# Kernel tuning notes

Measured on AMD Instinct MI355X. Metric: run time of the kernel, lower is better.

The kernel has to match this reference:

```python
import jax, jax.numpy as jnp
import numpy as np

N_NODES = 50000
N_EDGES = 800000
IN_DIM = 128
HID = 128
N_GRAPHS = 256
N_CLASSES = 2
ALPHA = 0.2  # leaky relu slope
EPS_BN = 1e-5


def setup_inputs() -> dict:
    key = jax.random.key(0)
    ks = jax.random.split(key, 24)
    adjacency = jax.random.randint(ks[0], (2, N_EDGES), 0, N_NODES, dtype=jnp.int32)
    input_feature = jax.random.normal(ks[1], (N_NODES, IN_DIM), dtype=jnp.float32)
    graph_indicator = jnp.sort(jax.random.randint(ks[2], (N_NODES,), 0, N_GRAPHS, dtype=jnp.int32))
    labels = jax.random.randint(ks[3], (N_GRAPHS,), 0, N_CLASSES, dtype=jnp.int64)
    s = 0.05
    params = {
        'W1': jax.random.normal(ks[4], (IN_DIM, HID), jnp.float32) * s,
        'a1': jax.random.normal(ks[5], (2 * HID,), jnp.float32) * s,
        'bn2_g': jnp.ones((HID,), jnp.float32),
        'bn2_b': jnp.zeros((HID,), jnp.float32),
        'W2': jax.random.normal(ks[6], (HID, HID), jnp.float32) * s,
        'a2': jax.random.normal(ks[7], (2 * HID,), jnp.float32) * s,
        'bn3_g': jnp.ones((HID,), jnp.float32),
        'bn3_b': jnp.zeros((HID,), jnp.float32),
        'W3': jax.random.normal(ks[8], (HID, HID), jnp.float32) * s,
        'a3': jax.random.normal(ks[9], (2 * HID,), jnp.float32) * s,
        'fc1_w': jax.random.normal(ks[10], (HID, 2 * HID), jnp.float32) * s,
        'fc1_b': jnp.zeros((2 * HID,), jnp.float32),
        'fc2_w': jax.random.normal(ks[11], (2 * HID, HID), jnp.float32) * s,
        'fc2_b': jnp.zeros((HID,), jnp.float32),
        'fc3_w': jax.random.normal(ks[12], (HID, N_CLASSES), jnp.float32) * s,
        'fc3_b': jnp.zeros((N_CLASSES,), jnp.float32),
    }
    return dict(adjacency=adjacency, input_feature=input_feature,
                graph_indicator=graph_indicator, labels=labels, **params)


def _batchnorm(x, g, b):
    # training-mode BatchNorm1d over node dim (biased variance)
    mu = jnp.mean(x, axis=0)
    var = jnp.mean((x - mu) ** 2, axis=0)
    return (x - mu) * jax.lax.rsqrt(var + EPS_BN) * g + b


def _sp_gat(x, src, dst, W, a):
    # pyGAT SpGraphAttentionLayer (dropout disabled / eval mode)
    h = x @ W                                # [N, F]
    F = h.shape[1]
    e_src = h @ a[:F]                        # [N]
    e_dst = h @ a[F:]                        # [N]
    e = e_src[src] + e_dst[dst]              # [E]
    ee = jnp.exp(-jax.nn.leaky_relu(e, ALPHA))
    rowsum = jax.ops.segment_sum(ee, src, num_segments=N_NODES)          # [N]
    num = jax.ops.segment_sum(ee[:, None] * h[dst], src, num_segments=N_NODES)  # [N, F]
    h_prime = num / (rowsum[:, None] + 1e-16)
    return jax.nn.elu(h_prime)


def reference(adjacency, input_feature, graph_indicator, labels,
              W1, a1, bn2_g, bn2_b, W2, a2, bn3_g, bn3_b, W3, a3,
              fc1_w, fc1_b, fc2_w, fc2_b, fc3_w, fc3_b):
    src, dst = adjacency[0], adjacency[1]
    # bn1 output is discarded in the original forward
    x = _sp_gat(input_feature, src, dst, W1, a1)
    x = _batchnorm(x, bn2_g, bn2_b)
    x = _sp_gat(x, src, dst, W2, a2)
    x = _batchnorm(x, bn3_g, bn3_b)
    x = _sp_gat(x, src, dst, W3, a3)
    # pooling_sum_4tensor: per-graph sum pooling
    pooled = jax.ops.segment_sum(x, graph_indicator, num_segments=N_GRAPHS)  # [G, F]
    x = jax.nn.relu(pooled @ fc1_w + fc1_b)
    x = jax.nn.relu(x @ fc2_w + fc2_b)
    logits = x @ fc3_w + fc3_b
    return logits
```

## Files before the change

### kernel.cpp

```cpp
#include <hip/hip_runtime.h>
#include <hip/hip_bf16.h>

#define N_NODES 50000
#define N_EDGES 800000
#define FD 128
#define N_GRAPHS 256
#define NPART 6250

typedef unsigned short u16;
typedef short bf16x8 __attribute__((ext_vector_type(8)));
typedef float f32x4 __attribute__((ext_vector_type(4)));

__device__ __forceinline__ u16 f2bf(float v) {
    __hip_bfloat16 h = __float2bfloat16(v);
    union { __hip_bfloat16 hh; u16 u; } c; c.hh = h; return c.u;
}
__device__ __forceinline__ float bf2f(u16 r) {
    return __uint_as_float(((unsigned int)r) << 16);
}

__global__ __launch_bounds__(256) void count_deg_part_k(const int* __restrict__ src,
                                                        int* __restrict__ cnt, int E) {
    int part = blockIdx.x & 7;
    int lo = part * NPART, hi = lo + NPART;
    int stride = (gridDim.x >> 3) * 256;
    for (int e = (blockIdx.x >> 3) * 256 + threadIdx.x; e < E; e += stride) {
        int s = src[e];
        if (s >= lo && s < hi) atomicAdd(&cnt[s], 1);
    }
}

__global__ __launch_bounds__(256) void fill_csr_part_k(const int* __restrict__ src,
                                                       const int* __restrict__ dst,
                                                       int* __restrict__ cur,
                                                       int2* __restrict__ epak, int E) {
    int part = blockIdx.x & 7;
    int lo = part * NPART, hi = lo + NPART;
    int stride = (gridDim.x >> 3) * 256;
    for (int e = (blockIdx.x >> 3) * 256 + threadIdx.x; e < E; e += stride) {
        int s = src[e];
        if (s >= lo && s < hi) {
            int p = atomicAdd(&cur[s], 1);
            epak[p].x = dst[e];
        }
    }
}

__global__ __launch_bounds__(256) void scan1_k(const int* __restrict__ cnt,
                                               int* __restrict__ bsum, int M) {
    int i = blockIdx.x * 256 + threadIdx.x;
    int v = (i < M) ? cnt[i] : 0;
    __shared__ int l[256];
    l[threadIdx.x] = v;
    __syncthreads();
    for (int s = 128; s > 0; s >>= 1) {
        if (threadIdx.x < s) l[threadIdx.x] += l[threadIdx.x + s];
        __syncthreads();
    }
    if (threadIdx.x == 0) bsum[blockIdx.x] = l[0];
}

__global__ __launch_bounds__(256) void scan2_k(int* __restrict__ bsum, int NB) {
    int tid = threadIdx.x;
    int v = (tid < NB) ? bsum[tid] : 0;
    __shared__ int l[256];
    l[tid] = v;
    __syncthreads();
    for (int off = 1; off < 256; off <<= 1) {
        int t = (tid >= off) ? l[tid - off] : 0;
        __syncthreads();
        l[tid] += t;
        __syncthreads();
    }
    if (tid < NB) bsum[tid] = l[tid] - v;
}

__global__ __launch_bounds__(256) void scan3_k(const int* __restrict__ cnt,
                                               const int* __restrict__ bsum,
                                               int* __restrict__ offs,
                                               int* __restrict__ cur, int M) {
    int i = blockIdx.x * 256 + threadIdx.x;
    int tid = threadIdx.x;
    int v = (i < M) ? cnt[i] : 0;
    __shared__ int l[256];
    l[tid] = v;
    __syncthreads();
    for (int off = 1; off < 256; off <<= 1) {
        int t = (tid >= off) ? l[tid - off] : 0;
        __syncthreads();
        l[tid] += t;
        __syncthreads();
    }
    int excl = l[tid] - v + bsum[blockIdx.x];
    if (i < M) { offs[i] = excl; cur[i] = excl; }
    if (i == M - 1) offs[M] = excl + v;
}

__global__ __launch_bounds__(256) void cvt_in_k(const float* __restrict__ X,
                                                u16* __restrict__ Xb, int n4) {
    int i = blockIdx.x * 256 + threadIdx.x;
    if (i < n4) {
        float4 v = ((const float4*)X)[i];
        ushort4 o;
        o.x = f2bf(v.x); o.y = f2bf(v.y); o.z = f2bf(v.z); o.w = f2bf(v.w);
        ((ushort4*)Xb)[i] = o;
    }
}

__global__ __launch_bounds__(128) void wprep_k(const float* __restrict__ W,
                                               const float* __restrict__ scale,
                                               const float* __restrict__ shift,
                                               u16* __restrict__ Wt,
                                               float* __restrict__ cvec) {
    int n = blockIdx.x, k = threadIdx.x;
    float w = W[(size_t)k * FD + n];
    Wt[(size_t)n * FD + k] = f2bf(scale[k] * w);
    __shared__ float l[128];
    l[k] = shift[k] * w;
    __syncthreads();
    for (int s = 64; s > 0; s >>= 1) {
        if (k < s) l[k] += l[k + s];
        __syncthreads();
    }
    if (k == 0) cvec[n] = l[0];
}

__global__ __launch_bounds__(256) void gemm_mfma_k(const u16* __restrict__ Xb,
                                                   const u16* __restrict__ Wt,
                                                   const float* __restrict__ cvec,
                                                   const float* __restrict__ avec,
                                                   u16* __restrict__ Hb,
                                                   float* __restrict__ es,
                                                   float* __restrict__ ed, int M) {
    __shared__ u16 As[64][136];
    __shared__ u16 Bs[128][136];
    __shared__ float sa_s[128], sa_d[128], cv[128];
    int tid = threadIdx.x;
    if (tid < 128) { sa_s[tid] = avec[tid]; sa_d[tid] = avec[128 + tid]; cv[tid] = cvec[tid]; }
    int row0 = blockIdx.x * 64;
    {
        int n = tid >> 1, k0 = (tid & 1) * 64;
        const uint4* s = (const uint4*)(Wt + (size_t)n * FD + k0);
#pragma unroll
        for (int u = 0; u < 8; u++) *(uint4*)&Bs[n][k0 + u * 8] = s[u];
    }
    {
        int r = tid >> 2, k0 = (tid & 3) * 32;
        int grow = row0 + r;
        if (grow < M) {
            const uint4* s = (const uint4*)(Xb + (size_t)grow * FD + k0);
#pragma unroll
            for (int u = 0; u < 4; u++) *(uint4*)&As[r][k0 + u * 8] = s[u];
        } else {
            uint4 z = make_uint4(0, 0, 0, 0);
#pragma unroll
            for (int u = 0; u < 4; u++) *(uint4*)&As[r][k0 + u * 8] = z;
        }
    }
    __syncthreads();

    int wave = tid >> 6, lane = tid & 63;
    int quad = lane >> 4, n16 = lane & 15;
    int rbase = wave * 16;
    f32x4 acc[8];
    f32x4 zz = {0.f, 0.f, 0.f, 0.f};
#pragma unroll
    for (int t = 0; t < 8; t++) acc[t] = zz;

#pragma unroll
    for (int kk = 0; kk < 128; kk += 32) {
        bf16x8 a = *(const bf16x8*)&As[rbase + n16][kk + quad * 8];
#pragma unroll
        for (int t = 0; t < 8; t++) {
            bf16x8 b = *(const bf16x8*)&Bs[t * 16 + n16][kk + quad * 8];
            acc[t] = __builtin_amdgcn_mfma_f32_16x16x32_bf16(a, b, acc[t], 0, 0, 0);
        }
    }

#pragma unroll
    for (int reg = 0; reg < 4; reg++) {
        int grow = row0 + rbase + quad * 4 + reg;
        float vals[8];
        float ps = 0.f, pd = 0.f;
#pragma unroll
        for (int t = 0; t < 8; t++) {
            float v = acc[t][reg] + cv[t * 16 + n16];
            vals[t] = v;
            ps += v * sa_s[t * 16 + n16];
            pd += v * sa_d[t * 16 + n16];
        }
#pragma unroll
        for (int o = 8; o > 0; o >>= 1) { ps += __shfl_xor(ps, o); pd += __shfl_xor(pd, o); }
        if (grow < M) {
            if (n16 == 0) { es[grow] = ps; ed[grow] = pd; }
#pragma unroll
            for (int t = 0; t < 8; t++)
                Hb[(size_t)grow * FD + t * 16 + n16] = f2bf(vals[t]);
        }
    }
}

__global__ __launch_bounds__(256) void ee_k(const float* __restrict__ es_,
                                            const float* __restrict__ ed_,
                                            const int* __restrict__ offs,
                                            int2* __restrict__ epak,
                                            float* __restrict__ rowsum, int M) {
    int wave = (blockIdx.x * blockDim.x + threadIdx.x) >> 6;
    int lane = threadIdx.x & 63;
    if (wave >= M) return;
    int s0 = offs[wave], s1 = offs[wave + 1];
    float es = es_[wave];
    float rs = 0.f;
    for (int base = s0; base < s1; base += 64) {
        int m = s1 - base; if (m > 64) m = 64;
        if (lane < m) {
            int d = epak[base + lane].x;
            float e = es + ed_[d];
            float lr = e > 0.f ? e : 0.2f * e;
            float v = __expf(-lr);
            epak[base + lane].y = __float_as_int(v);
            rs += v;
        }
    }
#pragma unroll
    for (int o = 32; o > 0; o >>= 1) rs += __shfl_xor(rs, o);
    if (lane == 0) rowsum[wave] = rs;
}

__global__ __launch_bounds__(256) void agg_k(const u16* __restrict__ Hb,
                                             const float* __restrict__ rowsum,
                                             const int* __restrict__ offs,
                                             const int2* __restrict__ epak,
                                             u16* __restrict__ OutB,
                                             float* __restrict__ OutF,
                                             int fp32out, int M) {
    int node = __builtin_amdgcn_readfirstlane((int)((blockIdx.x * blockDim.x + threadIdx.x) >> 6));
    int lane = threadIdx.x & 63;
    if (node >= M) return;
    int s0 = offs[node], s1 = offs[node + 1];
    const unsigned int* Hrow = (const unsigned int*)Hb;
    float2 a0 = make_float2(0.f, 0.f), a1 = make_float2(0.f, 0.f);
    int e = s0;
    for (; e + 4 <= s1; e += 4) {
        int2 p0 = epak[e];
        int2 p1 = epak[e + 1];
        int2 p2 = epak[e + 2];
        int2 p3 = epak[e + 3];
        unsigned int r0 = Hrow[(size_t)p0.x * 64 + lane];
        unsigned int r1 = Hrow[(size_t)p1.x * 64 + lane];
        unsigned int r2 = Hrow[(size_t)p2.x * 64 + lane];
        unsigned int r3 = Hrow[(size_t)p3.x * 64 + lane];
        float w0 = __int_as_float(p0.y), w1 = __int_as_float(p1.y);
        float w2 = __int_as_float(p2.y), w3 = __int_as_float(p3.y);
        a0.x += w0 * __int_as_float(r0 << 16);
        a0.y += w0 * __int_as_float(r0 & 0xffff0000u);
        a1.x += w1 * __int_as_float(r1 << 16);
        a1.y += w1 * __int_as_float(r1 & 0xffff0000u);
        a0.x += w2 * __int_as_float(r2 << 16);
        a0.y += w2 * __int_as_float(r2 & 0xffff0000u);
        a1.x += w3 * __int_as_float(r3 << 16);
        a1.y += w3 * __int_as_float(r3 & 0xffff0000u);
    }
    for (; e < s1; e++) {
        int2 p = epak[e];
        unsigned int r = Hrow[(size_t)p.x * 64 + lane];
        float w = __int_as_float(p.y);
        a0.x += w * __int_as_float(r << 16);
        a0.y += w * __int_as_float(r & 0xffff0000u);
    }
    float inv = 1.f / (rowsum[node] + 1e-16f);
    float vx = (a0.x + a1.x) * inv;
    float vy = (a0.y + a1.y) * inv;
    vx = vx > 0.f ? vx : (__expf(vx) - 1.f);
    vy = vy > 0.f ? vy : (__expf(vy) - 1.f);
    if (fp32out) {
        ((float2*)OutF)[(size_t)node * 64 + lane] = make_float2(vx, vy);
    } else {
        unsigned int pk = ((unsigned int)f2bf(vy) << 16) | f2bf(vx);
        ((unsigned int*)OutB)[(size_t)node * 64 + lane] = pk;
    }
}

__global__ void bnstats_b_k(const u16* __restrict__ Xb, float* __restrict__ sums,
                            float* __restrict__ sumsq, int M) {
    int f = threadIdx.x & 127;
    int half = threadIdx.x >> 7;
    float s1 = 0.f, s2 = 0.f;
    for (int r = blockIdx.x * 2 + half; r < M; r += gridDim.x * 2) {
        float v = bf2f(Xb[(size_t)r * FD + f]);
        s1 += v; s2 += v * v;
    }
    __shared__ float l1[256], l2[256];
    l1[threadIdx.x] = s1; l2[threadIdx.x] = s2;
    __syncthreads();
    if (half == 0) {
        atomicAdd(&sums[f], l1[f] + l1[f + 128]);
        atomicAdd(&sumsq[f], l2[f] + l2[f + 128]);
    }
}

__global__ void init_affine_k(float* scale, float* shift, float* sums, float* sumsq) {
    int f = threadIdx.x;
    scale[f] = 1.f; shift[f] = 0.f; sums[f] = 0.f; sumsq[f] = 0.f;
}

__global__ void bnfinal_k(float* sums, float* sumsq, const float* __restrict__ g,
                          const float* __restrict__ b, float* scale, float* shift, float invN) {
    int f = threadIdx.x;
    float mu = sums[f] * invN;
    float var = sumsq[f] * invN - mu * mu;
    float sc = g[f] * rsqrtf(var + 1e-5f);
    scale[f] = sc;
    shift[f] = b[f] - mu * sc;
    sums[f] = 0.f; sumsq[f] = 0.f;
}

__global__ void pool_k(const float* __restrict__ X, const int* __restrict__ gi,
                       float* __restrict__ pooled, int M) {
    int f = threadIdx.x & 127;
    int half = threadIdx.x >> 7;
    int r0 = blockIdx.x * 128 + half;
    int rend = min(blockIdx.x * 128 + 128, M);
    int curg = -1; float acc = 0.f;
    for (int r = r0; r < rend; r += 2) {
        int g = gi[r];
        if (g != curg) {
            if (curg >= 0) atomicAdd(&pooled[(size_t)curg * FD + f], acc);
            curg = g; acc = 0.f;
        }
        acc += X[(size_t)r * FD + f];
    }
    if (curg >= 0) atomicAdd(&pooled[(size_t)curg * FD + f], acc);
}

__global__ void fc_relu_k(const float* __restrict__ X, const float* __restrict__ Wt,
                          const float* __restrict__ b, float* __restrict__ Y,
                          int K, int Ncols) {
    int g = blockIdx.x;
    int j = threadIdx.x;
    extern __shared__ float xrow[];
    for (int k = threadIdx.x; k < K; k += blockDim.x) xrow[k] = X[(size_t)g * K + k];
    __syncthreads();
    float s = b[j];
    for (int k = 0; k < K; k++) s += xrow[k] * Wt[(size_t)k * Ncols + j];
    Y[(size_t)g * Ncols + j] = fmaxf(s, 0.f);
}

__global__ void fc3_k(const float* __restrict__ X, const float* __restrict__ W,
                      const float* __restrict__ b, float* __restrict__ out) {
    int g = blockIdx.x;
    int l = threadIdx.x;
    float2 x2 = ((const float2*)X)[g * 64 + l];
    float s0 = x2.x * W[(2 * l) * 2]     + x2.y * W[(2 * l + 1) * 2];
    float s1 = x2.x * W[(2 * l) * 2 + 1] + x2.y * W[(2 * l + 1) * 2 + 1];
#pragma unroll
    for (int o = 32; o > 0; o >>= 1) { s0 += __shfl_xor(s0, o); s1 += __shfl_xor(s1, o); }
    if (l == 0) { out[g * 2] = s0 + b[0]; out[g * 2 + 1] = s1 + b[1]; }
}

extern "C" void kernel_launch(void* const* d_in, const int* in_sizes, int n_in,
                              void* d_out, int out_size, void* d_ws, size_t ws_size,
                              hipStream_t stream) {
    const int*   adj  = (const int*)d_in[0];
    const float* xin  = (const float*)d_in[1];
    const int*   gi   = (const int*)d_in[2];
    const float* W1   = (const float*)d_in[4];
    const float* a1   = (const float*)d_in[5];
    const float* bn2g = (const float*)d_in[6];
    const float* bn2b = (const float*)d_in[7];
    const float* W2   = (const float*)d_in[8];
    const float* a2   = (const float*)d_in[9];
    const float* bn3g = (const float*)d_in[10];
    const float* bn3b = (const float*)d_in[11];
    const float* W3   = (const float*)d_in[12];
    const float* a3   = (const float*)d_in[13];
    const float* fc1w = (const float*)d_in[14];
    const float* fc1b = (const float*)d_in[15];
    const float* fc2w = (const float*)d_in[16];
    const float* fc2b = (const float*)d_in[17];
    const float* fc3w = (const float*)d_in[18];
    const float* fc3b = (const float*)d_in[19];
    float* out = (float*)d_out;

    const int N = N_NODES, E = N_EDGES, G = N_GRAPHS;

    float* buf1   = (float*)d_ws;
    u16*   Xb     = (u16*)(buf1 + (size_t)N * FD);
    u16*   Hb     = Xb + (size_t)N * FD;
    u16*   Wt     = Hb + (size_t)N * FD;
    float* es     = (float*)(Wt + FD * FD);
    float* ed     = es + N;
    float* rowsum = ed + N;
    float* scale  = rowsum + N;
    float* shift  = scale + FD;
    float* sums   = shift + FD;
    float* sumsq  = sums + FD;
    float* cvec   = sumsq + FD;
    float* pooled = cvec + FD;
    float* t1     = pooled + (size_t)G * FD;
    float* t2     = t1 + (size_t)G * 256;
    int*   degcnt = (int*)(t2 + (size_t)G * FD);
    int*   offs   = degcnt + N;
    int*   cur    = offs + (N + 2);
    int*   bsum   = cur + N;
    int2*  epak   = (int2*)(bsum + 256);

    const int* srcp = adj;
    const int* dstp = adj + E;

    const int NB = (N + 255) / 256;

    hipMemsetAsync(degcnt, 0, (size_t)N * sizeof(int), stream);
    count_deg_part_k<<<8 * 392, 256, 0, stream>>>(srcp, degcnt, E);
    scan1_k<<<NB, 256, 0, stream>>>(degcnt, bsum, N);
    scan2_k<<<1, 256, 0, stream>>>(bsum, NB);
    scan3_k<<<NB, 256, 0, stream>>>(degcnt, bsum, offs, cur, N);
    fill_csr_part_k<<<8 * 392, 256, 0, stream>>>(srcp, dstp, cur, epak, E);
    init_affine_k<<<1, 128, 0, stream>>>(scale, shift, sums, sumsq);
    cvt_in_k<<<(N * FD / 4 + 255) / 256, 256, 0, stream>>>(xin, Xb, N * FD / 4);

    const int gemm_grid = (N + 63) / 64;
    const int wave_grid = (N + 3) / 4;
    const float invN = 1.0f / (float)N;

    wprep_k<<<FD, 128, 0, stream>>>(W1, scale, shift, Wt, cvec);
    gemm_mfma_k<<<gemm_grid, 256, 0, stream>>>(Xb, Wt, cvec, a1, Hb, es, ed, N);
    ee_k<<<wave_grid, 256, 0, stream>>>(es, ed, offs, epak, rowsum, N);
    agg_k<<<wave_grid, 256, 0, stream>>>(Hb, rowsum, offs, epak, Xb, buf1, 0, N);
    bnstats_b_k<<<256, 256, 0, stream>>>(Xb, sums, sumsq, N);
    bnfinal_k<<<1, 128, 0, stream>>>(sums, sumsq, bn2g, bn2b, scale, shift, invN);

    wprep_k<<<FD, 128, 0, stream>>>(W2, scale, shift, Wt, cvec);
    gemm_mfma_k<<<gemm_grid, 256, 0, stream>>>(Xb, Wt, cvec, a2, Hb, es, ed, N);
    ee_k<<<wave_grid, 256, 0, stream>>>(es, ed, offs, epak, rowsum, N);
    agg_k<<<wave_grid, 256, 0, stream>>>(Hb, rowsum, offs, epak, Xb, buf1, 0, N);
    bnstats_b_k<<<256, 256, 0, stream>>>(Xb, sums, sumsq, N);
    bnfinal_k<<<1, 128, 0, stream>>>(sums, sumsq, bn3g, bn3b, scale, shift, invN);

    wprep_k<<<FD, 128, 0, stream>>>(W3, scale, shift, Wt, cvec);
    gemm_mfma_k<<<gemm_grid, 256, 0, stream>>>(Xb, Wt, cvec, a3, Hb, es, ed, N);
    ee_k<<<wave_grid, 256, 0, stream>>>(es, ed, offs, epak, rowsum, N);
    agg_k<<<wave_grid, 256, 0, stream>>>(Hb, rowsum, offs, epak, Xb, buf1, 1, N);

    hipMemsetAsync(pooled, 0, (size_t)G * FD * sizeof(float), stream);
    pool_k<<<(N + 127) / 128, 256, 0, stream>>>(buf1, gi, pooled, N);
    fc_relu_k<<<G, 256, FD * sizeof(float), stream>>>(pooled, fc1w, fc1b, t1, FD, 256);
    fc_relu_k<<<G, 128, 256 * sizeof(float), stream>>>(t1, fc2w, fc2b, t2, 256, FD);
    fc3_k<<<G, 64, 0, stream>>>(t2, fc3w, fc3b, out);
}
```

Before: 494.2 us.

## Fuse edge-weight computation into aggregation kernel and drop packed edge weights

Removes the separate ee_k pass. agg_k now computes each edge's attention weight inline from es/ed and accumulates the row sum in-register, so the edge array shrinks from int2 to int and the rowsum buffer is gone. The aggregation loop is unrolled to 8 edges with 4 accumulators, and edge indices are made wave-uniform via readfirstlane. This cuts a kernel launch and the edge-array read/write traffic per layer. In exchange, every lane redundantly computes the exp and loads ed for each edge.

```diff
diff --git a/kernel.cpp b/kernel.cpp
--- a/kernel.cpp
+++ b/kernel.cpp
@@ -33,7 +33,7 @@
 __global__ __launch_bounds__(256) void fill_csr_part_k(const int* __restrict__ src,
                                                        const int* __restrict__ dst,
                                                        int* __restrict__ cur,
-                                                       int2* __restrict__ epak, int E) {
+                                                       int* __restrict__ edst, int E) {
     int part = blockIdx.x & 7;
     int lo = part * NPART, hi = lo + NPART;
     int stride = (gridDim.x >> 3) * 256;
@@ -41,7 +41,7 @@
         int s = src[e];
         if (s >= lo && s < hi) {
             int p = atomicAdd(&cur[s], 1);
-            epak[p].x = dst[e];
+            edst[p] = dst[e];
         }
     }
 }
@@ -200,37 +200,11 @@
     }
 }
 
-__global__ __launch_bounds__(256) void ee_k(const float* __restrict__ es_,
-                                            const float* __restrict__ ed_,
-                                            const int* __restrict__ offs,
-                                            int2* __restrict__ epak,
-                                            float* __restrict__ rowsum, int M) {
-    int wave = (blockIdx.x * blockDim.x + threadIdx.x) >> 6;
-    int lane = threadIdx.x & 63;
-    if (wave >= M) return;
-    int s0 = offs[wave], s1 = offs[wave + 1];
-    float es = es_[wave];
-    float rs = 0.f;
-    for (int base = s0; base < s1; base += 64) {
-        int m = s1 - base; if (m > 64) m = 64;
-        if (lane < m) {
-            int d = epak[base + lane].x;
-            float e = es + ed_[d];
-            float lr = e > 0.f ? e : 0.2f * e;
-            float v = __expf(-lr);
-            epak[base + lane].y = __float_as_int(v);
-            rs += v;
-        }
-    }
-#pragma unroll
-    for (int o = 32; o > 0; o >>= 1) rs += __shfl_xor(rs, o);
-    if (lane == 0) rowsum[wave] = rs;
-}
-
 __global__ __launch_bounds__(256) void agg_k(const u16* __restrict__ Hb,
-                                             const float* __restrict__ rowsum,
+                                             const float* __restrict__ es_,
+                                             const float* __restrict__ ed_,
                                              const int* __restrict__ offs,
-                                             const int2* __restrict__ epak,
+                                             const int* __restrict__ edst,
                                              u16* __restrict__ OutB,
                                              float* __restrict__ OutF,
                                              int fp32out, int M) {
@@ -238,39 +212,47 @@
     int lane = threadIdx.x & 63;
     if (node >= M) return;
     int s0 = offs[node], s1 = offs[node + 1];
+    float esv = es_[node];
     const unsigned int* Hrow = (const unsigned int*)Hb;
     float2 a0 = make_float2(0.f, 0.f), a1 = make_float2(0.f, 0.f);
+    float2 a2 = make_float2(0.f, 0.f), a3 = make_float2(0.f, 0.f);
+    float rs = 0.f;
     int e = s0;
-    for (; e + 4 <= s1; e += 4) {
-        int2 p0 = epak[e];
-        int2 p1 = epak[e + 1];
-        int2 p2 = epak[e + 2];
-        int2 p3 = epak[e + 3];
-        unsigned int r0 = Hrow[(size_t)p0.x * 64 + lane];
-        unsigned int r1 = Hrow[(size_t)p1.x * 64 + lane];
-        unsigned int r2 = Hrow[(size_t)p2.x * 64 + lane];
-        unsigned int r3 = Hrow[(size_t)p3.x * 64 + lane];
-        float w0 = __int_as_float(p0.y), w1 = __int_as_float(p1.y);
-        float w2 = __int_as_float(p2.y), w3 = __int_as_float(p3.y);
-        a0.x += w0 * __int_as_float(r0 << 16);
-        a0.y += w0 * __int_as_float(r0 & 0xffff0000u);
-        a1.x += w1 * __int_as_float(r1 << 16);
-        a1.y += w1 * __int_as_float(r1 & 0xffff0000u);
-        a0.x += w2 * __int_as_float(r2 << 16);
-        a0.y += w2 * __int_as_float(r2 & 0xffff0000u);
-        a1.x += w3 * __int_as_float(r3 << 16);
-        a1.y += w3 * __int_as_float(r3 & 0xffff0000u);
+    for (; e + 8 <= s1; e += 8) {
+        int d[8];
+#pragma unroll
+        for (int u = 0; u < 8; u++) d[u] = __builtin_amdgcn_readfirstlane(edst[e + u]);
+        float w[8];
+#pragma unroll
+        for (int u = 0; u < 8; u++) {
+            float ev = esv + ed_[d[u]];
+            float lr = ev > 0.f ? ev : 0.2f * ev;
+            w[u] = __expf(-lr);
+        }
+        unsigned int r[8];
+#pragma unroll
+        for (int u = 0; u < 8; u++) r[u] = Hrow[(size_t)d[u] * 64 + lane];
+#pragma unroll
+        for (int u = 0; u < 8; u++) {
+            rs += w[u];
+            float2* ac = (u & 3) == 0 ? &a0 : (u & 3) == 1 ? &a1 : (u & 3) == 2 ? &a2 : &a3;
+            ac->x += w[u] * __int_as_float(r[u] << 16);
+            ac->y += w[u] * __int_as_float(r[u] & 0xffff0000u);
+        }
     }
     for (; e < s1; e++) {
-        int2 p = epak[e];
-        unsigned int r = Hrow[(size_t)p.x * 64 + lane];
-        float w = __int_as_float(p.y);
-        a0.x += w * __int_as_float(r << 16);
-        a0.y += w * __int_as_float(r & 0xffff0000u);
-    }
-    float inv = 1.f / (rowsum[node] + 1e-16f);
-    float vx = (a0.x + a1.x) * inv;
-    float vy = (a0.y + a1.y) * inv;
+        int d = __builtin_amdgcn_readfirstlane(edst[e]);
+        float ev = esv + ed_[d];
+        float lr = ev > 0.f ? ev : 0.2f * ev;
+        float wv = __expf(-lr);
+        rs += wv;
+        unsigned int r = Hrow[(size_t)d * 64 + lane];
+        a0.x += wv * __int_as_float(r << 16);
+        a0.y += wv * __int_as_float(r & 0xffff0000u);
+    }
+    float inv = 1.f / (rs + 1e-16f);
+    float vx = (a0.x + a1.x + a2.x + a3.x) * inv;
+    float vy = (a0.y + a1.y + a2.y + a3.y) * inv;
     vx = vx > 0.f ? vx : (__expf(vx) - 1.f);
     vy = vy > 0.f ? vy : (__expf(vy) - 1.f);
     if (fp32out) {
@@ -390,8 +372,7 @@
     u16*   Wt     = Hb + (size_t)N * FD;
     float* es     = (float*)(Wt + FD * FD);
     float* ed     = es + N;
-    float* rowsum = ed + N;
-    float* scale  = rowsum + N;
+    float* scale  = ed + N;
     float* shift  = scale + FD;
     float* sums   = shift + FD;
     float* sumsq  = sums + FD;
@@ -403,7 +384,7 @@
     int*   offs   = degcnt + N;
     int*   cur    = offs + (N + 2);
     int*   bsum   = cur + N;
-    int2*  epak   = (int2*)(bsum + 256);
+    int*   edst   = bsum + 256;
 
     const int* srcp = adj;
     const int* dstp = adj + E;
@@ -415,7 +396,7 @@
     scan1_k<<<NB, 256, 0, stream>>>(degcnt, bsum, N);
     scan2_k<<<1, 256, 0, stream>>>(bsum, NB);
     scan3_k<<<NB, 256, 0, stream>>>(degcnt, bsum, offs, cur, N);
-    fill_csr_part_k<<<8 * 392, 256, 0, stream>>>(srcp, dstp, cur, epak, E);
+    fill_csr_part_k<<<8 * 392, 256, 0, stream>>>(srcp, dstp, cur, edst, E);
     init_affine_k<<<1, 128, 0, stream>>>(scale, shift, sums, sumsq);
     cvt_in_k<<<(N * FD / 4 + 255) / 256, 256, 0, stream>>>(xin, Xb, N * FD / 4);
 
@@ -425,22 +406,19 @@
 
     wprep_k<<<FD, 128, 0, stream>>>(W1, scale, shift, Wt, cvec);
     gemm_mfma_k<<<gemm_grid, 256, 0, stream>>>(Xb, Wt, cvec, a1, Hb, es, ed, N);
-    ee_k<<<wave_grid, 256, 0, stream>>>(es, ed, offs, epak, rowsum, N);
-    agg_k<<<wave_grid, 256, 0, stream>>>(Hb, rowsum, offs, epak, Xb, buf1, 0, N);
+    agg_k<<<wave_grid, 256, 0, stream>>>(Hb, es, ed, offs, edst, Xb, buf1, 0, N);
     bnstats_b_k<<<256, 256, 0, stream>>>(Xb, sums, sumsq, N);
     bnfinal_k<<<1, 128, 0, stream>>>(sums, sumsq, bn2g, bn2b, scale, shift, invN);
 
     wprep_k<<<FD, 128, 0, stream>>>(W2, scale, shift, Wt, cvec);
     gemm_mfma_k<<<gemm_grid, 256, 0, stream>>>(Xb, Wt, cvec, a2, Hb, es, ed, N);
-    ee_k<<<wave_grid, 256, 0, stream>>>(es, ed, offs, epak, rowsum, N);
-    agg_k<<<wave_grid, 256, 0, stream>>>(Hb, rowsum, offs, epak, Xb, buf1, 0, N);
+    agg_k<<<wave_grid, 256, 0, stream>>>(Hb, es, ed, offs, edst, Xb, buf1, 0, N);
     bnstats_b_k<<<256, 256, 0, stream>>>(Xb, sums, sumsq, N);
     bnfinal_k<<<1, 128, 0, stream>>>(sums, sumsq, bn3g, bn3b, scale, shift, invN);
 
     wprep_k<<<FD, 128, 0, stream>>>(W3, scale, shift, Wt, cvec);
     gemm_mfma_k<<<gemm_grid, 256, 0, stream>>>(Xb, Wt, cvec, a3, Hb, es, ed, N);
-    ee_k<<<wave_grid, 256, 0, stream>>>(es, ed, offs, epak, rowsum, N);
-    agg_k<<<wave_grid, 256, 0, stream>>>(Hb, rowsum, offs, epak, Xb, buf1, 1, N);
+    agg_k<<<wave_grid, 256, 0, stream>>>(Hb, es, ed, offs, edst, Xb, buf1, 1, N);
 
     hipMemsetAsync(pooled, 0, (size_t)G * FD * sizeof(float), stream);
     pool_k<<<(N + 127) / 128, 256, 0, stream>>>(buf1, gi, pooled, N);
```

Result: faster. 459.3 us (-7.1%).
